# Optimization experiments

Measured on AMD Instinct MI355X. Metric: run time of the kernel, lower is better.

The kernel has to match this reference:

```python
import jax, jax.numpy as jnp
import numpy as np

B, DIN, F, H, C = 8192, 2048, 2048, 2048, 345
EPS = 1e-5


def setup_inputs() -> dict:
    key = jax.random.key(0)
    ks = jax.random.split(key, 8)
    rng = np.random.default_rng(0)
    # labels and sort order (torch.sort is stable here via argsort kind='stable')
    y_np = rng.integers(0, C, size=B).astype(np.int64)
    order_np = np.argsort(y_np, kind='stable')
    ys = y_np[order_np]
    # per-class random permutations within each sorted segment (torch.randperm per interval)
    shuf1 = np.empty(B, dtype=np.int64)
    shuf2 = np.empty(B, dtype=np.int64)
    for c in np.unique(ys):
        idx = np.nonzero(ys == c)[0]
        shuf1[idx] = rng.permutation(idx)
        shuf2[idx] = rng.permutation(idx)
    s = 0.02  # weight init scale
    return {
        'x': jax.random.normal(ks[0], (B, DIN), jnp.float32),
        'lam': jnp.array([float(rng.beta(0.5, 0.5))], jnp.float32),
        'Wf': jax.random.normal(ks[1], (DIN, F), jnp.float32) * s,
        'bf': jnp.zeros((F,), jnp.float32),
        'W1': jax.random.normal(ks[2], (F, H), jnp.float32) * s,
        'b1': jnp.zeros((H,), jnp.float32),
        'g1': jnp.ones((H,), jnp.float32),
        'be1': jnp.zeros((H,), jnp.float32),
        'W2': jax.random.normal(ks[3], (H, H), jnp.float32) * s,
        'b2': jnp.zeros((H,), jnp.float32),
        'g2': jnp.ones((H,), jnp.float32),
        'be2': jnp.zeros((H,), jnp.float32),
        'W3': jax.random.normal(ks[4], (H, F), jnp.float32) * s,
        'b3': jnp.zeros((F,), jnp.float32),
        'g3': jnp.ones((F,), jnp.float32),
        'be3': jnp.zeros((F,), jnp.float32),
        'Wc': jax.random.normal(ks[5], (F, C), jnp.float32) * s,
        'bc': jnp.zeros((C,), jnp.float32),
        'y': jnp.asarray(y_np),
        'order': jnp.asarray(order_np),
        'shuf1': jnp.asarray(shuf1),
        'shuf2': jnp.asarray(shuf2),
    }


def _bn(x, g, b):
    # BatchNorm1d, training mode: biased batch stats
    m = jnp.mean(x, axis=0)
    v = jnp.var(x, axis=0)
    return (x - m) * jax.lax.rsqrt(v + EPS) * g + b


def reference(x, lam, Wf, bf, W1, b1, g1, be1, W2, b2, g2, be2, W3, b3, g3, be3, Wc, bc, y, order, shuf1, shuf2):
    lam = lam[0]
    xs = x[order]           # sorted-by-label gather (vectorized)
    ys = y[order]
    feat = jax.nn.relu(xs @ Wf + bf)                      # featurizer
    h = jax.nn.relu(_bn(feat @ W1 + b1, g1, be1))         # cdpl projector
    h = jax.nn.relu(_bn(h @ W2 + b2, g2, be2))
    proj = _bn(h @ W3 + b3, g3, be3)
    out = feat @ Wc + bc                                  # classifier logits
    out2, feat2 = out[shuf1], proj[shuf1]                 # per-class shuffles
    out3, feat3 = out[shuf2], proj[shuf2]
    out3 = lam * out2 + (1.0 - lam) * out3
    feat3 = lam * feat2 + (1.0 - lam) * feat3
    mse = lambda a, b: jnp.mean((a - b) ** 2)
    L_ind_logit = mse(out, out2)
    L_hdl_logit = mse(out, out3)
    L_ind_feat = 0.3 * mse(proj, feat2)
    L_hdl_feat = 0.3 * mse(proj, feat3)
    logp = jax.nn.log_softmax(out, axis=-1)
    cl_loss = -jnp.mean(jnp.take_along_axis(logp, ys[:, None], axis=-1))
    C_scale = jax.lax.stop_gradient(jnp.minimum(cl_loss, 1.0))  # .item() -> constant
    loss = cl_loss + C_scale * (lam * (L_ind_logit + L_ind_feat) + (1.0 - lam) * (L_hdl_logit + L_hdl_feat))
    return loss
```

## Files before the change

kernel.cpp:

```cpp
#include <hip/hip_runtime.h>

#define NB   8192
#define NF   2048
#define NC   345
#define NCP  384
#define EPSV 1e-5f

#define SX   (5.75f / 127.0f)
#define SW   (0.115f / 127.0f)
#define SF   (5.2f / 127.0f)
#define SH   (5.75f / 127.0f)
#define QX   (1.0f / SX)
#define QW   (1.0f / SW)
#define QF   (1.0f / SF)
#define QH   (1.0f / SH)

typedef __bf16 bf16x8 __attribute__((ext_vector_type(8)));
typedef float  f32x4  __attribute__((ext_vector_type(4)));
typedef int    i32x4  __attribute__((ext_vector_type(4)));

__device__ __forceinline__ float bs2f(unsigned int u) { return __uint_as_float(u << 16); }
__device__ __forceinline__ unsigned short f2bs(float f) {
    unsigned int u = __float_as_uint(f);
    u += 0x7fffu + ((u >> 16) & 1u);
    return (unsigned short)(u >> 16);
}
__device__ __forceinline__ int q8i(float v, float iq) {
    int t = __float2int_rn(v * iq);
    return t > 127 ? 127 : (t < -127 ? -127 : t);
}

#define GLD16(g, l)                                                                     \
    __builtin_amdgcn_global_load_lds((const __attribute__((address_space(1))) void*)(g),\
                                     (__attribute__((address_space(3))) void*)(l),      \
                                     16, 0, 0)

__global__ void k_gather(const float* __restrict__ x, const int* __restrict__ order,
                         char* __restrict__ xq) {
    const int row = blockIdx.x;
    const long src = order[row];
    const float4* xr = (const float4*)(x + src * 2048);
    float4 a = xr[threadIdx.x * 2 + 0];
    float4 b = xr[threadIdx.x * 2 + 1];
    unsigned int lo = (unsigned)(q8i(a.x, QX) & 255) | ((unsigned)(q8i(a.y, QX) & 255) << 8) |
                      ((unsigned)(q8i(a.z, QX) & 255) << 16) | ((unsigned)(q8i(a.w, QX) & 255) << 24);
    unsigned int hi = (unsigned)(q8i(b.x, QX) & 255) | ((unsigned)(q8i(b.y, QX) & 255) << 8) |
                      ((unsigned)(q8i(b.z, QX) & 255) << 16) | ((unsigned)(q8i(b.w, QX) & 255) << 24);
    uint2 o; o.x = lo; o.y = hi;
    ((uint2*)(xq + (long)row * 2048))[threadIdx.x] = o;
}

template <int Q8>
__global__ void k_transpose(const float* __restrict__ W, char* __restrict__ Wt8,
                            unsigned short* __restrict__ Wtb, int K, int N, int Npad) {
    __shared__ float tile[32][33];
    const int n0 = blockIdx.x * 32, k0 = blockIdx.y * 32;
    const int tx = threadIdx.x, ty = threadIdx.y;
    #pragma unroll
    for (int i = 0; i < 32; i += 8) {
        int n = n0 + tx, k = k0 + ty + i;
        tile[ty + i][tx] = (n < N) ? W[(long)k * N + n] : 0.f;
    }
    __syncthreads();
    #pragma unroll
    for (int i = 0; i < 32; i += 8) {
        int n = n0 + ty + i, k = k0 + tx;
        if (n < Npad) {
            if (Q8) Wt8[(long)n * K + k] = (char)q8i(tile[tx][ty + i], QW);
            else    Wtb[(long)n * K + k] = f2bs(tile[tx][ty + i]);
        }
    }
}

#define BARX  do { asm volatile("" ::: "memory"); __builtin_amdgcn_s_barrier(); \
                   asm volatile("" ::: "memory"); } while (0)
#define VMW4  asm volatile("s_waitcnt vmcnt(4)" ::: "memory")
#define VMW0  asm volatile("s_waitcnt vmcnt(0)" ::: "memory")

#define RDX(u, AV, BV) do {                                                            \
    const char* A_ = &L[((u) & 3) * 32768];                                            \
    const char* B_ = A_ + 16384;                                                       \
    _Pragma("unroll") for (int m_ = 0; m_ < 8; m_++)                                   \
        AV[m_] = *(const i32x4*)&A_[(wm * 128 + m_ * 16 + frow) * 64 + slt];           \
    _Pragma("unroll") for (int n_ = 0; n_ < 4; n_++)                                   \
        BV[n_] = *(const i32x4*)&B_[(wn * 64 + n_ * 16 + frow) * 64 + slt];            \
} while (0)

#define MMX(AV, BV) do {                                                               \
    __builtin_amdgcn_s_setprio(1);                                                     \
    _Pragma("unroll") for (int n_ = 0; n_ < 4; n_++)                                   \
    _Pragma("unroll") for (int m_ = 0; m_ < 8; m_++)                                   \
        acc[m_][n_] = __builtin_amdgcn_mfma_i32_16x16x64_i8(BV[n_], AV[m_],            \
                                                            acc[m_][n_], 0, 0, 0);    \
    __builtin_amdgcn_s_setprio(0);                                                     \
} while (0)

template <int RELU, int STATS, int I8OUT>
__global__ __launch_bounds__(512, 2) void k_gemmq(
    const char* __restrict__ A,
    const char* __restrict__ Bt,
    const float* __restrict__ bias,
    unsigned short* __restrict__ Cb,
    char* __restrict__ C8,
    float* __restrict__ stats,
    float S, float IQ, int N, int K) {
    __shared__ char L[4 * 32768];
    const int tid  = threadIdx.x;
    const int lane = tid & 63;
    const int wv   = tid >> 6;
    const int frow = lane & 15;
    const int kg   = lane >> 4;
    const int wm   = wv >> 2;
    const int wn   = wv & 3;
    const int slt  = (kg ^ ((frow >> 1) & 3)) * 16;

    const int id  = blockIdx.x;
    const int xcd = id & 7, kid = id >> 3;
    const int brow = (xcd * 4 + (kid & 3)) * 256;
    const int bcol = (kid >> 2) * 256;

    const char* pA[2];
    const char* pB[2];
    #pragma unroll
    for (int i = 0; i < 2; i++) {
        const int q = tid + i * 512;
        const int j = q >> 2;
        const int c = (q & 3) ^ ((j >> 1) & 3);
        pA[i] = A  + (long)(brow + j) * K + c * 16;
        pB[i] = Bt + (long)(bcol + j) * K + c * 16;
    }

    i32x4 acc[8][4];
    #pragma unroll
    for (int m = 0; m < 8; m++)
        #pragma unroll
        for (int n = 0; n < 4; n++)
            #pragma unroll
            for (int r = 0; r < 4; r++) acc[m][n][r] = 0;

    auto stage = [&](int s) {
        char* Lb = &L[(s & 3) * 32768];
        const int ko = s * 64;
        GLD16(pA[0] + ko, Lb + wv * 1024);
        GLD16(pA[1] + ko, Lb + 8192 + wv * 1024);
        GLD16(pB[0] + ko, Lb + 16384 + wv * 1024);
        GLD16(pB[1] + ko, Lb + 24576 + wv * 1024);
    };

    i32x4 avA[8], bvA[4], avB[8], bvB[4];

    stage(0); stage(1); stage(2);
    VMW4; BARX;
    RDX(0, avA, bvA);

    for (int i = 0; i < 14; i++) {
        const int t = i * 2;
        RDX(t + 1, avB, bvB); stage(t + 3); MMX(avA, bvA); VMW4; BARX;
        RDX(t + 2, avA, bvA); stage(t + 4); MMX(avB, bvB); VMW4; BARX;
    }
    RDX(29, avB, bvB); stage(31); MMX(avA, bvA); VMW4; BARX;
    RDX(30, avA, bvA); MMX(avB, bvB); VMW0; BARX;
    RDX(31, avB, bvB); MMX(avA, bvA);
    MMX(avB, bvB);

    const int rbase = brow + wm * 128 + frow;
    const int cbase = bcol + wn * 64 + kg * 4;
    #pragma unroll
    for (int n = 0; n < 4; n++) {
        const int col = cbase + n * 16;
        const float4 bb = *(const float4*)&bias[col];
        float s0_ = 0.f, s1_ = 0.f, s2_ = 0.f, s3_ = 0.f;
        float q0_ = 0.f, q1_ = 0.f, q2_ = 0.f, q3_ = 0.f;
        #pragma unroll
        for (int m = 0; m < 8; m++) {
            const long row = rbase + m * 16;
            float v0 = (float)acc[m][n][0] * S + bb.x;
            float v1 = (float)acc[m][n][1] * S + bb.y;
            float v2 = (float)acc[m][n][2] * S + bb.z;
            float v3 = (float)acc[m][n][3] * S + bb.w;
            if (STATS) { s0_ += v0; q0_ += v0 * v0; s1_ += v1; q1_ += v1 * v1;
                         s2_ += v2; q2_ += v2 * v2; s3_ += v3; q3_ += v3 * v3; }
            if (RELU) { v0 = fmaxf(v0, 0.f); v1 = fmaxf(v1, 0.f);
                        v2 = fmaxf(v2, 0.f); v3 = fmaxf(v3, 0.f); }
            ushort4 st; st.x = f2bs(v0); st.y = f2bs(v1); st.z = f2bs(v2); st.w = f2bs(v3);
            *(ushort4*)&Cb[row * N + col] = st;
            if (I8OUT) {
                unsigned int p = (unsigned)(q8i(v0, IQ) & 255) |
                                 ((unsigned)(q8i(v1, IQ) & 255) << 8) |
                                 ((unsigned)(q8i(v2, IQ) & 255) << 16) |
                                 ((unsigned)(q8i(v3, IQ) & 255) << 24);
                *(unsigned int*)&C8[row * N + col] = p;
            }
        }
        if (STATS) {
            #pragma unroll
            for (int off = 1; off <= 8; off <<= 1) {
                s0_ += __shfl_xor(s0_, off); s1_ += __shfl_xor(s1_, off);
                s2_ += __shfl_xor(s2_, off); s3_ += __shfl_xor(s3_, off);
                q0_ += __shfl_xor(q0_, off); q1_ += __shfl_xor(q1_, off);
                q2_ += __shfl_xor(q2_, off); q3_ += __shfl_xor(q3_, off);
            }
            if (frow == 0) {
                atomicAdd(&stats[col + 0], s0_); atomicAdd(&stats[col + 1], s1_);
                atomicAdd(&stats[col + 2], s2_); atomicAdd(&stats[col + 3], s3_);
                atomicAdd(&stats[N + col + 0], q0_); atomicAdd(&stats[N + col + 1], q1_);
                atomicAdd(&stats[N + col + 2], q2_); atomicAdd(&stats[N + col + 3], q3_);
            }
        }
    }
}

__global__ __launch_bounds__(256) void k_gemm(const unsigned short* __restrict__ A,
                                              const unsigned short* __restrict__ Bt,
                                              const float* __restrict__ bias,
                                              float* __restrict__ Cf,
                                              int M, int N, int K, int ldc) {
    constexpr int BK = 64;
    __shared__ unsigned short As[128 * BK];
    __shared__ unsigned short Bs[128 * BK];
    const int tid  = threadIdx.x;
    const int lane = tid & 63;
    const int wv   = tid >> 6;
    const int brow = blockIdx.x * 128;
    const int bcol = blockIdx.y * 128;
    const int wr   = (wv >> 1) * 64;
    const int wc   = (wv & 1) * 64;
    const int frow = lane & 15;
    const int kg   = lane >> 4;
    const int rx   = frow & 7;
    const int srow  = lane >> 3;
    const int sslot = (lane & 7) ^ srow;

    f32x4 acc[4][4];
    #pragma unroll
    for (int m = 0; m < 4; m++)
        #pragma unroll
        for (int n = 0; n < 4; n++)
            #pragma unroll
            for (int r = 0; r < 4; r++) acc[m][n][r] = 0.f;

    for (int kt = 0; kt < K; kt += BK) {
        #pragma unroll
        for (int i = 0; i < 4; i++) {
            const int c = wv * 4 + i;
            const int r = c * 8 + srow;
            GLD16(A + (long)(brow + r) * K + kt + sslot * 8, &As[c * 512]);
        }
        #pragma unroll
        for (int i = 0; i < 4; i++) {
            const int c = wv * 4 + i;
            const int r = c * 8 + srow;
            GLD16(Bt + (long)(bcol + r) * K + kt + sslot * 8, &Bs[c * 512]);
        }
        __syncthreads();
        #pragma unroll
        for (int kk = 0; kk < 2; kk++) {
            bf16x8 av[4], bv[4];
            #pragma unroll
            for (int m = 0; m < 4; m++) {
                const int row = wr + m * 16 + frow;
                av[m] = *(const bf16x8*)&As[row * BK + (((kk * 4 + kg) ^ rx) * 8)];
            }
            #pragma unroll
            for (int n = 0; n < 4; n++) {
                const int row = wc + n * 16 + frow;
                bv[n] = *(const bf16x8*)&Bs[row * BK + (((kk * 4 + kg) ^ rx) * 8)];
            }
            #pragma unroll
            for (int m = 0; m < 4; m++)
                #pragma unroll
                for (int n = 0; n < 4; n++)
                    acc[m][n] = __builtin_amdgcn_mfma_f32_16x16x32_bf16(av[m], bv[n],
                                                                        acc[m][n], 0, 0, 0);
        }
        __syncthreads();
    }
    const int r0 = brow + wr + (lane >> 4) * 4;
    const int c0 = bcol + wc + (lane & 15);
    #pragma unroll
    for (int n = 0; n < 4; n++) {
        const int col = c0 + n * 16;
        if (col < N) {
            const float bb = bias[col];
            #pragma unroll
            for (int m = 0; m < 4; m++)
                #pragma unroll
                for (int r = 0; r < 4; r++) {
                    const int row = r0 + m * 16 + r;
                    Cf[(long)row * ldc + col] = acc[m][n][r] + bb;
                }
        }
    }
}

__global__ void k_bnfin(float* __restrict__ sums, const float* __restrict__ g,
                        const float* __restrict__ be, int ncols) {
    const int c = blockIdx.x * blockDim.x + threadIdx.x;
    const float m   = sums[c] * (1.f / NB);
    const float var = sums[ncols + c] * (1.f / NB) - m * m;
    const float sc  = rsqrtf(var + EPSV) * g[c];
    sums[c] = sc;
    sums[ncols + c] = be[c] - m * sc;
}

__global__ void k_bnapplyq(const unsigned short* __restrict__ t, const float* __restrict__ sums,
                           char* __restrict__ o8, int ncols) {
    const long i  = ((long)blockIdx.x * blockDim.x + threadIdx.x) * 8;
    const int  c0 = (int)(i & (ncols - 1));
    uint4 v = *(const uint4*)(t + i);
    unsigned int us[8] = {v.x & 0xffffu, v.x >> 16, v.y & 0xffffu, v.y >> 16,
                          v.z & 0xffffu, v.z >> 16, v.w & 0xffffu, v.w >> 16};
    unsigned int b[8];
    #pragma unroll
    for (int j = 0; j < 8; j++) {
        const int c = c0 + j;
        float val = bs2f(us[j]) * sums[c] + sums[ncols + c];
        val = fmaxf(val, 0.f);
        b[j] = (unsigned)(q8i(val, QH) & 255);
    }
    uint2 o;
    o.x = b[0] | (b[1] << 8) | (b[2] << 16) | (b[3] << 24);
    o.y = b[4] | (b[5] << 8) | (b[6] << 16) | (b[7] << 24);
    *(uint2*)(o8 + i) = o;
}

__global__ __launch_bounds__(256) void k_logitloss(const float* __restrict__ out,
                            const int* __restrict__ y,
                            const int* __restrict__ order, const int* __restrict__ s1,
                            const int* __restrict__ s2, const float* __restrict__ lamp,
                            float* __restrict__ acc) {
    const int lane = threadIdx.x & 63;
    const int wv   = threadIdx.x >> 6;
    const int wid  = blockIdx.x * 4 + wv;
    const int nw   = gridDim.x * 4;
    const float lam = lamp[0];
    float ce = 0.f, d1 = 0.f, d2 = 0.f;
    for (int i = wid; i < NB; i += nw) {
        const float* o  = out + (long)i * NCP;
        const float* o2 = out + (long)s1[i] * NCP;
        const float* o3 = out + (long)s2[i] * NCP;
        float v[6];
        float mx = -1e30f;
        #pragma unroll
        for (int j = 0; j < 6; j++) {
            const int c = lane + j * 64;
            if (c < NC) {
                const float a = o[c], b = o2[c], cc = o3[c];
                const float mix = lam * b + (1.f - lam) * cc;
                v[j] = a;
                d1 += (a - b) * (a - b);
                d2 += (a - mix) * (a - mix);
                mx = fmaxf(mx, a);
            } else v[j] = -1e30f;
        }
        #pragma unroll
        for (int off = 32; off; off >>= 1) mx = fmaxf(mx, __shfl_xor(mx, off));
        float se = 0.f;
        #pragma unroll
        for (int j = 0; j < 6; j++) se += expf(v[j] - mx);
        #pragma unroll
        for (int off = 32; off; off >>= 1) se += __shfl_xor(se, off);
        if (lane == 0) {
            const int yv = y[order[i]];
            ce += mx + logf(se) - o[yv];
        }
    }
    #pragma unroll
    for (int off = 32; off; off >>= 1) {
        d1 += __shfl_xor(d1, off);
        d2 += __shfl_xor(d2, off);
    }
    __shared__ float red[4][3];
    if (lane == 0) { red[wv][0] = ce; red[wv][1] = d1; red[wv][2] = d2; }
    __syncthreads();
    if (threadIdx.x == 0) {
        atomicAdd(&acc[0], red[0][0] + red[1][0] + red[2][0] + red[3][0]);
        atomicAdd(&acc[1], red[0][1] + red[1][1] + red[2][1] + red[3][1]);
        atomicAdd(&acc[2], red[0][2] + red[1][2] + red[2][2] + red[3][2]);
    }
}

__global__ __launch_bounds__(256) void k_featloss(const unsigned short* __restrict__ t3,
                           const float* __restrict__ st,
                           const int* __restrict__ s1,
                           const int* __restrict__ s2, const float* __restrict__ lamp,
                           float* __restrict__ acc) {
    const int t = threadIdx.x;
    const float lam = lamp[0];
    float sc[8], sh[8];
    #pragma unroll
    for (int j = 0; j < 8; j++) { sc[j] = st[t * 8 + j]; sh[j] = st[NF + t * 8 + j]; }
    float d1 = 0.f, d2 = 0.f;
    for (int i = blockIdx.x; i < NB; i += gridDim.x) {
        uint4 a = ((const uint4*)(t3 + (long)i * NF))[t];
        uint4 b = ((const uint4*)(t3 + (long)s1[i] * NF))[t];
        uint4 c = ((const uint4*)(t3 + (long)s2[i] * NF))[t];
        unsigned int ua[8] = {a.x & 0xffffu, a.x >> 16, a.y & 0xffffu, a.y >> 16,
                              a.z & 0xffffu, a.z >> 16, a.w & 0xffffu, a.w >> 16};
        unsigned int ub[8] = {b.x & 0xffffu, b.x >> 16, b.y & 0xffffu, b.y >> 16,
                              b.z & 0xffffu, b.z >> 16, b.w & 0xffffu, b.w >> 16};
        unsigned int uc[8] = {c.x & 0xffffu, c.x >> 16, c.y & 0xffffu, c.y >> 16,
                              c.z & 0xffffu, c.z >> 16, c.w & 0xffffu, c.w >> 16};
        #pragma unroll
        for (int j = 0; j < 8; j++) {
            float pa = sc[j] * bs2f(ua[j]) + sh[j];
            float pb = sc[j] * bs2f(ub[j]) + sh[j];
            float pc = sc[j] * bs2f(uc[j]) + sh[j];
            float mix = lam * pb + (1.f - lam) * pc;
            d1 += (pa - pb) * (pa - pb);
            d2 += (pa - mix) * (pa - mix);
        }
    }
    #pragma unroll
    for (int off = 32; off; off >>= 1) {
        d1 += __shfl_xor(d1, off);
        d2 += __shfl_xor(d2, off);
    }
    __shared__ float r1[4], r2[4];
    if ((t & 63) == 0) { r1[t >> 6] = d1; r2[t >> 6] = d2; }
    __syncthreads();
    if (t == 0) {
        atomicAdd(&acc[3], r1[0] + r1[1] + r1[2] + r1[3]);
        atomicAdd(&acc[4], r2[0] + r2[1] + r2[2] + r2[3]);
    }
}

__global__ void k_final(const float* __restrict__ acc, const float* __restrict__ lamp,
                        float* __restrict__ outp) {
    const float lam = lamp[0];
    const float cl  = acc[0] * (1.f / NB);
    const float Lil = acc[1] * (1.f / ((float)NB * NC));
    const float Lhl = acc[2] * (1.f / ((float)NB * NC));
    const float Lif = 0.3f * acc[3] * (1.f / ((float)NB * NF));
    const float Lhf = 0.3f * acc[4] * (1.f / ((float)NB * NF));
    const float Cs  = fminf(cl, 1.f);
    outp[0] = cl + Cs * (lam * (Lil + Lif) + (1.f - lam) * (Lhl + Lhf));
}

extern "C" void kernel_launch(void* const* d_in, const int* in_sizes, int n_in,
                              void* d_out, int out_size, void* d_ws, size_t ws_size,
                              hipStream_t stream) {
    const float* x   = (const float*)d_in[0];
    const float* lam = (const float*)d_in[1];
    const float* Wf  = (const float*)d_in[2];
    const float* bf_ = (const float*)d_in[3];
    const float* W1  = (const float*)d_in[4];
    const float* b1  = (const float*)d_in[5];
    const float* g1  = (const float*)d_in[6];
    const float* be1 = (const float*)d_in[7];
    const float* W2  = (const float*)d_in[8];
    const float* b2  = (const float*)d_in[9];
    const float* g2  = (const float*)d_in[10];
    const float* be2 = (const float*)d_in[11];
    const float* W3  = (const float*)d_in[12];
    const float* b3  = (const float*)d_in[13];
    const float* g3  = (const float*)d_in[14];
    const float* be3 = (const float*)d_in[15];
    const float* Wc  = (const float*)d_in[16];
    const float* bc  = (const float*)d_in[17];
    const int* y     = (const int*)d_in[18];
    const int* order = (const int*)d_in[19];
    const int* s1    = (const int*)d_in[20];
    const int* s2    = (const int*)d_in[21];
    float* outp = (float*)d_out;

    char* ws = (char*)d_ws;
    const size_t MB = 1024 * 1024;
    char*           R0  = ws;
    unsigned short* R0b = (unsigned short*)R0;
    char*           R1  = ws + 32 * MB;
    unsigned short* R1b = (unsigned short*)R1;
    char*           R2  = ws + 64 * MB;
    char*           R3  = ws + 80 * MB;
    float*          outbuf = (float*)(ws + 96 * MB);
    char*           WT0 = ws + 108 * MB;
    char*           WT1 = ws + 112 * MB;
    char*           WT2 = ws + 116 * MB;
    char*           WT3 = ws + 120 * MB;
    unsigned short* WCT = (unsigned short*)(ws + 124 * MB);
    float* stats = (float*)(ws + 126 * MB);
    float* accs  = stats + 3 * 4096;

    hipMemsetAsync(stats, 0, (3 * 4096 + 8) * sizeof(float), stream);

    dim3 tb(32, 8);
    k_transpose<1><<<dim3(64, 64), tb, 0, stream>>>(Wf, WT0, nullptr, 2048, 2048, 2048);
    k_transpose<1><<<dim3(64, 64), tb, 0, stream>>>(W1, WT1, nullptr, 2048, 2048, 2048);
    k_transpose<1><<<dim3(64, 64), tb, 0, stream>>>(W2, WT2, nullptr, 2048, 2048, 2048);
    k_transpose<1><<<dim3(64, 64), tb, 0, stream>>>(W3, WT3, nullptr, 2048, 2048, 2048);
    k_transpose<0><<<dim3(12, 64), tb, 0, stream>>>(Wc, nullptr, WCT, 2048, NC, NCP);

    k_gather<<<NB, 256, 0, stream>>>(x, order, R0);

    k_gemmq<1, 0, 1><<<256, 512, 0, stream>>>(R0, WT0, bf_, R1b, R2, nullptr,
                                              SX * SW, QF, 2048, 2048);
    k_gemm<<<dim3(64, 3), 256, 0, stream>>>(R1b, WCT, bc, outbuf, NB, NC, 2048, NCP);
    k_gemmq<0, 1, 0><<<256, 512, 0, stream>>>(R2, WT1, b1, R0b, nullptr, stats,
                                              SF * SW, 0.f, 2048, 2048);
    k_bnfin<<<8, 256, 0, stream>>>(stats, g1, be1, 2048);
    k_bnapplyq<<<8192, 256, 0, stream>>>(R0b, stats, R3, 2048);
    k_gemmq<0, 1, 0><<<256, 512, 0, stream>>>(R3, WT2, b2, R0b, nullptr, stats + 4096,
                                              SH * SW, 0.f, 2048, 2048);
    k_bnfin<<<8, 256, 0, stream>>>(stats + 4096, g2, be2, 2048);
    k_bnapplyq<<<8192, 256, 0, stream>>>(R0b, stats + 4096, R2, 2048);
    k_gemmq<0, 1, 0><<<256, 512, 0, stream>>>(R2, WT3, b3, R1b, nullptr, stats + 8192,
                                              SH * SW, 0.f, 2048, 2048);
    k_bnfin<<<8, 256, 0, stream>>>(stats + 8192, g3, be3, 2048);

    k_logitloss<<<512, 256, 0, stream>>>(outbuf, y, order, s1, s2, lam, accs);
    k_featloss<<<512, 256, 0, stream>>>(R1b, stats + 8192, s1, s2, lam, accs);
    k_final<<<1, 1, 0, stream>>>(accs, lam, outp);
}
```

Before: 346.5 us.

## Stage GEMM epilogue through LDS and store pre-BN activations as int8

The int8 GEMM epilogue now writes bf16 results into swizzled shared memory and then emits coalesced 16-byte row stores, optionally as bf16 and/or int8. The pre-BatchNorm intermediates of layers 1 and 2 are stored as int8 with fixed scales instead of bf16, so the BN-apply kernels read half the bytes. The classifier GEMM switches to vectorized float4 epilogue stores using a padded bias. The goal is less HBM traffic and better store coalescing. The cost is an extra quantization step with hardcoded ranges that only fit the expected activation magnitudes, which adds accuracy risk.

```diff
diff --git a/kernel.cpp b/kernel.cpp
--- a/kernel.cpp
+++ b/kernel.cpp
@@ -10,10 +10,14 @@
 #define SW   (0.115f / 127.0f)
 #define SF   (5.2f / 127.0f)
 #define SH   (5.75f / 127.0f)
+#define ST1  (3.34f / 127.0f)
+#define ST2  (3.68f / 127.0f)
 #define QX   (1.0f / SX)
 #define QW   (1.0f / SW)
 #define QF   (1.0f / SF)
 #define QH   (1.0f / SH)
+#define QT1  (1.0f / ST1)
+#define QT2  (1.0f / ST2)
 
 typedef __bf16 bf16x8 __attribute__((ext_vector_type(8)));
 typedef float  f32x4  __attribute__((ext_vector_type(4)));
@@ -72,8 +76,14 @@
     }
 }
 
+__global__ void k_padbias(const float* __restrict__ bc, float* __restrict__ bcp) {
+    const int i = threadIdx.x + blockIdx.x * blockDim.x;
+    if (i < NCP) bcp[i] = (i < NC) ? bc[i] : 0.f;
+}
+
 #define BARX  do { asm volatile("" ::: "memory"); __builtin_amdgcn_s_barrier(); \
                    asm volatile("" ::: "memory"); } while (0)
+#define LGKM0 asm volatile("s_waitcnt lgkmcnt(0)" ::: "memory")
 #define VMW4  asm volatile("s_waitcnt vmcnt(4)" ::: "memory")
 #define VMW0  asm volatile("s_waitcnt vmcnt(0)" ::: "memory")
 
@@ -95,7 +105,7 @@
     __builtin_amdgcn_s_setprio(0);                                                     \
 } while (0)
 
-template <int RELU, int STATS, int I8OUT>
+template <int RELU, int STATS, int B16OUT, int I8OUT>
 __global__ __launch_bounds__(512, 2) void k_gemmq(
     const char* __restrict__ A,
     const char* __restrict__ Bt,
@@ -163,7 +173,8 @@
     RDX(31, avB, bvB); MMX(avA, bvA);
     MMX(avB, bvB);
 
-    const int rbase = brow + wm * 128 + frow;
+    LGKM0; BARX;
+    unsigned short* Ls = (unsigned short*)L;
     const int cbase = bcol + wn * 64 + kg * 4;
     #pragma unroll
     for (int n = 0; n < 4; n++) {
@@ -171,9 +182,11 @@
         const float4 bb = *(const float4*)&bias[col];
         float s0_ = 0.f, s1_ = 0.f, s2_ = 0.f, s3_ = 0.f;
         float q0_ = 0.f, q1_ = 0.f, q2_ = 0.f, q3_ = 0.f;
+        const int s8 = wn * 16 + n * 4 + kg;
+        const int p8 = s8 ^ frow;
         #pragma unroll
         for (int m = 0; m < 8; m++) {
-            const long row = rbase + m * 16;
+            const int rloc = wm * 128 + m * 16 + frow;
             float v0 = (float)acc[m][n][0] * S + bb.x;
             float v1 = (float)acc[m][n][1] * S + bb.y;
             float v2 = (float)acc[m][n][2] * S + bb.z;
@@ -183,14 +196,7 @@
             if (RELU) { v0 = fmaxf(v0, 0.f); v1 = fmaxf(v1, 0.f);
                         v2 = fmaxf(v2, 0.f); v3 = fmaxf(v3, 0.f); }
             ushort4 st; st.x = f2bs(v0); st.y = f2bs(v1); st.z = f2bs(v2); st.w = f2bs(v3);
-            *(ushort4*)&Cb[row * N + col] = st;
-            if (I8OUT) {
-                unsigned int p = (unsigned)(q8i(v0, IQ) & 255) |
-                                 ((unsigned)(q8i(v1, IQ) & 255) << 8) |
-                                 ((unsigned)(q8i(v2, IQ) & 255) << 16) |
-                                 ((unsigned)(q8i(v3, IQ) & 255) << 24);
-                *(unsigned int*)&C8[row * N + col] = p;
-            }
+            *(ushort4*)&Ls[rloc * 256 + p8 * 4] = st;
         }
         if (STATS) {
             #pragma unroll
@@ -206,6 +212,31 @@
                 atomicAdd(&stats[N + col + 0], q0_); atomicAdd(&stats[N + col + 1], q1_);
                 atomicAdd(&stats[N + col + 2], q2_); atomicAdd(&stats[N + col + 3], q3_);
             }
+        }
+    }
+    LGKM0; BARX;
+    #pragma unroll
+    for (int it = 0; it < 16; it++) {
+        const int c  = tid + it * 512;
+        const int r  = c >> 5;
+        const int a  = c & 31;
+        const int x  = r & 15;
+        const int a2 = a ^ (x >> 1);
+        uint4 v = *(const uint4*)&Ls[r * 256 + a2 * 8];
+        if (x & 1) { unsigned tx_ = v.x, ty_ = v.y; v.x = v.z; v.y = v.w; v.z = tx_; v.w = ty_; }
+        const long grow = brow + r;
+        const int  gcol = bcol + a * 8;
+        if (B16OUT) *(uint4*)&Cb[grow * N + gcol] = v;
+        if (I8OUT) {
+            unsigned int us[8] = {v.x & 0xffffu, v.x >> 16, v.y & 0xffffu, v.y >> 16,
+                                  v.z & 0xffffu, v.z >> 16, v.w & 0xffffu, v.w >> 16};
+            unsigned int b[8];
+            #pragma unroll
+            for (int j = 0; j < 8; j++) b[j] = (unsigned)(q8i(bs2f(us[j]), IQ) & 255);
+            uint2 o;
+            o.x = b[0] | (b[1] << 8) | (b[2] << 16) | (b[3] << 24);
+            o.y = b[4] | (b[5] << 8) | (b[6] << 16) | (b[7] << 24);
+            *(uint2*)&C8[grow * N + gcol] = o;
         }
     }
 }
@@ -270,25 +301,24 @@
             for (int m = 0; m < 4; m++)
                 #pragma unroll
                 for (int n = 0; n < 4; n++)
-                    acc[m][n] = __builtin_amdgcn_mfma_f32_16x16x32_bf16(av[m], bv[n],
+                    acc[m][n] = __builtin_amdgcn_mfma_f32_16x16x32_bf16(bv[n], av[m],
                                                                         acc[m][n], 0, 0, 0);
         }
         __syncthreads();
     }
-    const int r0 = brow + wr + (lane >> 4) * 4;
-    const int c0 = bcol + wc + (lane & 15);
+    const int r0 = brow + wr + frow;
+    const int c0 = bcol + wc + kg * 4;
     #pragma unroll
     for (int n = 0; n < 4; n++) {
         const int col = c0 + n * 16;
-        if (col < N) {
-            const float bb = bias[col];
-            #pragma unroll
-            for (int m = 0; m < 4; m++)
-                #pragma unroll
-                for (int r = 0; r < 4; r++) {
-                    const int row = r0 + m * 16 + r;
-                    Cf[(long)row * ldc + col] = acc[m][n][r] + bb;
-                }
+        const float4 bb = *(const float4*)&bias[col];
+        #pragma unroll
+        for (int m = 0; m < 4; m++) {
+            const long row = r0 + m * 16;
+            float4 o;
+            o.x = acc[m][n][0] + bb.x; o.y = acc[m][n][1] + bb.y;
+            o.z = acc[m][n][2] + bb.z; o.w = acc[m][n][3] + bb.w;
+            *(float4*)&Cf[row * ldc + col] = o;
         }
     }
 }
@@ -303,18 +333,18 @@
     sums[ncols + c] = be[c] - m * sc;
 }
 
-__global__ void k_bnapplyq(const unsigned short* __restrict__ t, const float* __restrict__ sums,
-                           char* __restrict__ o8, int ncols) {
+__global__ void k_bnapplyq8(const char* __restrict__ t8, const float* __restrict__ sums,
+                            char* __restrict__ o8, float St, int ncols) {
     const long i  = ((long)blockIdx.x * blockDim.x + threadIdx.x) * 8;
     const int  c0 = (int)(i & (ncols - 1));
-    uint4 v = *(const uint4*)(t + i);
-    unsigned int us[8] = {v.x & 0xffffu, v.x >> 16, v.y & 0xffffu, v.y >> 16,
-                          v.z & 0xffffu, v.z >> 16, v.w & 0xffffu, v.w >> 16};
+    uint2 v = *(const uint2*)(t8 + i);
     unsigned int b[8];
     #pragma unroll
     for (int j = 0; j < 8; j++) {
+        const unsigned int w = (j < 4) ? v.x : v.y;
+        const int raw = (int)(signed char)((w >> ((j & 3) * 8)) & 0xffu);
         const int c = c0 + j;
-        float val = bs2f(us[j]) * sums[c] + sums[ncols + c];
+        float val = (float)raw * St * sums[c] + sums[ncols + c];
         val = fmaxf(val, 0.f);
         b[j] = (unsigned)(q8i(val, QH) & 255);
     }
@@ -467,19 +497,19 @@
     char* ws = (char*)d_ws;
     const size_t MB = 1024 * 1024;
     char*           R0  = ws;
-    unsigned short* R0b = (unsigned short*)R0;
-    char*           R1  = ws + 32 * MB;
+    char*           R1  = ws + 16 * MB;
     unsigned short* R1b = (unsigned short*)R1;
-    char*           R2  = ws + 64 * MB;
-    char*           R3  = ws + 80 * MB;
-    float*          outbuf = (float*)(ws + 96 * MB);
-    char*           WT0 = ws + 108 * MB;
-    char*           WT1 = ws + 112 * MB;
-    char*           WT2 = ws + 116 * MB;
-    char*           WT3 = ws + 120 * MB;
-    unsigned short* WCT = (unsigned short*)(ws + 124 * MB);
-    float* stats = (float*)(ws + 126 * MB);
+    char*           R2  = ws + 48 * MB;
+    char*           R3  = ws + 64 * MB;
+    float*          outbuf = (float*)(ws + 80 * MB);
+    char*           WT0 = ws + 92 * MB;
+    char*           WT1 = ws + 96 * MB;
+    char*           WT2 = ws + 100 * MB;
+    char*           WT3 = ws + 104 * MB;
+    unsigned short* WCT = (unsigned short*)(ws + 108 * MB);
+    float* stats = (float*)(ws + 110 * MB);
     float* accs  = stats + 3 * 4096;
+    float* bcp   = accs + 16;
 
     hipMemsetAsync(stats, 0, (3 * 4096 + 8) * sizeof(float), stream);
 
@@ -489,22 +519,23 @@
     k_transpose<1><<<dim3(64, 64), tb, 0, stream>>>(W2, WT2, nullptr, 2048, 2048, 2048);
     k_transpose<1><<<dim3(64, 64), tb, 0, stream>>>(W3, WT3, nullptr, 2048, 2048, 2048);
     k_transpose<0><<<dim3(12, 64), tb, 0, stream>>>(Wc, nullptr, WCT, 2048, NC, NCP);
+    k_padbias<<<2, 192, 0, stream>>>(bc, bcp);
 
     k_gather<<<NB, 256, 0, stream>>>(x, order, R0);
 
-    k_gemmq<1, 0, 1><<<256, 512, 0, stream>>>(R0, WT0, bf_, R1b, R2, nullptr,
-                                              SX * SW, QF, 2048, 2048);
-    k_gemm<<<dim3(64, 3), 256, 0, stream>>>(R1b, WCT, bc, outbuf, NB, NC, 2048, NCP);
-    k_gemmq<0, 1, 0><<<256, 512, 0, stream>>>(R2, WT1, b1, R0b, nullptr, stats,
-                                              SF * SW, 0.f, 2048, 2048);
+    k_gemmq<1, 0, 1, 1><<<256, 512, 0, stream>>>(R0, WT0, bf_, R1b, R2, nullptr,
+                                                 SX * SW, QF, 2048, 2048);
+    k_gemm<<<dim3(64, 3), 256, 0, stream>>>(R1b, WCT, bcp, outbuf, NB, NC, 2048, NCP);
+    k_gemmq<0, 1, 0, 1><<<256, 512, 0, stream>>>(R2, WT1, b1, nullptr, R3, stats,
+                                                 SF * SW, QT1, 2048, 2048);
     k_bnfin<<<8, 256, 0, stream>>>(stats, g1, be1, 2048);
-    k_bnapplyq<<<8192, 256, 0, stream>>>(R0b, stats, R3, 2048);
-    k_gemmq<0, 1, 0><<<256, 512, 0, stream>>>(R3, WT2, b2, R0b, nullptr, stats + 4096,
-                                              SH * SW, 0.f, 2048, 2048);
+    k_bnapplyq8<<<8192, 256, 0, stream>>>(R3, stats, R0, ST1, 2048);
+    k_gemmq<0, 1, 0, 1><<<256, 512, 0, stream>>>(R0, WT2, b2, nullptr, R3, stats + 4096,
+                                                 SH * SW, QT2, 2048, 2048);
     k_bnfin<<<8, 256, 0, stream>>>(stats + 4096, g2, be2, 2048);
-    k_bnapplyq<<<8192, 256, 0, stream>>>(R0b, stats + 4096, R2, 2048);
-    k_gemmq<0, 1, 0><<<256, 512, 0, stream>>>(R2, WT3, b3, R1b, nullptr, stats + 8192,
-                                              SH * SW, 0.f, 2048, 2048);
+    k_bnapplyq8<<<8192, 256, 0, stream>>>(R3, stats + 4096, R2, ST2, 2048);
+    k_gemmq<0, 1, 1, 0><<<256, 512, 0, stream>>>(R2, WT3, b3, R1b, nullptr, stats + 8192,
+                                                 SH * SW, 0.f, 2048, 2048);
     k_bnfin<<<8, 256, 0, stream>>>(stats + 8192, g3, be3, 2048);
 
     k_logitloss<<<512, 256, 0, stream>>>(outbuf, y, order, s1, s2, lam, accs);
```

After: 325.5 us. 1.06x faster.
